# Optimization experiments

Measured on AMD Instinct MI355X. Metric: run time of the kernel, lower is better.

Reference implementation:

```python
import jax, jax.numpy as jnp
import numpy as np

DIM = 1024
HEADS = 8  # hardcoded in original view(batch, N, 3, 8, -1)
HEAD_DIM = DIM // HEADS
# NOTE: original computes self.d = (dim/head_num)**(-0.5) and then divides scores by it,
# which is equivalent to MULTIPLYING scores by sqrt(head_dim). We replicate that exactly.
SCALE = float(np.sqrt(DIM / HEADS))


def setup_inputs() -> dict:
    key = jax.random.key(0)
    k_x, k_w1, k_b1, k_w0, k_b0 = jax.random.split(key, 5)
    B, N = 4, 2048
    bound1 = 1.0 / np.sqrt(DIM)
    x = jax.random.normal(k_x, (B, N, DIM), dtype=jnp.float32)
    # nn.Linear(dim, dim*3): weight [3*dim, dim], bias [3*dim]
    W_qkv = jax.random.uniform(k_w1, (3 * DIM, DIM), jnp.float32, -bound1, bound1)
    b_qkv = jax.random.uniform(k_b1, (3 * DIM,), jnp.float32, -bound1, bound1)
    # nn.Linear(dim, dim)
    W0 = jax.random.uniform(k_w0, (DIM, DIM), jnp.float32, -bound1, bound1)
    b0 = jax.random.uniform(k_b0, (DIM,), jnp.float32, -bound1, bound1)
    return {"x": x, "W_qkv": W_qkv, "b_qkv": b_qkv, "W0": W0, "b0": b0}


def reference(x, W_qkv, b_qkv, W0, b0):
    B, N, C = x.shape
    qkv = jnp.einsum("bnc,oc->bno", x, W_qkv) + b_qkv          # [B,N,3C]
    qkv = qkv.reshape(B, N, 3, HEADS, HEAD_DIM)
    qkv = jnp.transpose(qkv, (2, 0, 3, 1, 4))                   # [3,B,H,N,Dh]
    q, k, v = qkv[0], qkv[1], qkv[2]
    scores = jnp.einsum("bhnd,bhmd->bhnm", q, k) * SCALE        # [B,H,N,N]
    attn = jax.nn.softmax(scores, axis=-1)
    out = jnp.einsum("bhnm,bhmd->bhnd", attn, v)                # [B,H,N,Dh]
    out = jnp.transpose(out, (0, 2, 1, 3)).reshape(B, N, C)
    return jnp.einsum("bnc,oc->bno", out, W0) + b0
```

## Files before the change

### kernel.cpp

```cpp
#include <hip/hip_runtime.h>
#include <hip/hip_bf16.h>

constexpr int DIM   = 1024;
constexpr int HEADS = 8;
constexpr int HD    = 128;
constexpr int SEQ   = 2048;
constexpr int BATCH = 4;
constexpr int BN_ROWS = BATCH * SEQ;
#define SCALE_F 11.3137084989847603904f

typedef __attribute__((ext_vector_type(8))) short  short8;
typedef __attribute__((ext_vector_type(8))) ushort u16x8;
typedef __attribute__((ext_vector_type(4))) float  f32x4;

__device__ __forceinline__ ushort split_hi(float x, float& rem) {
    unsigned xb = __builtin_bit_cast(unsigned, x);
    unsigned hb = xb & 0xFFFF0000u;
    rem = x - __builtin_bit_cast(float, hb);
    return (ushort)(xb >> 16);
}
__device__ __forceinline__ ushort rne16(float x) {
    unsigned xb = __builtin_bit_cast(unsigned, x);
    unsigned r  = xb + 0x7FFFu + ((xb >> 16) & 1u);
    return (ushort)(r >> 16);
}

constexpr int GS = 40;

__global__ __launch_bounds__(256)
void gemm_split_kernel(const float* __restrict__ A, const float* __restrict__ B,
                       const float* __restrict__ bias, float* __restrict__ C,
                       int M, int N, int K)
{
    __shared__ ushort Ah[128 * GS], Al[128 * GS];
    __shared__ ushort Bh[128 * GS], Bl[128 * GS];

    const int tid  = threadIdx.x;
    const int lane = tid & 63;
    const int w    = tid >> 6;
    const int l15  = lane & 15;
    const int g    = lane >> 4;

    const int nbn   = N >> 7;
    const int nb    = (M >> 7) * nbn;
    const int chunk = nb >> 3;
    const int pid   = blockIdx.x;
    const int lb    = (pid & 7) * chunk + (pid >> 3);
    const int m0    = (lb / nbn) * 128;
    const int n0    = (lb % nbn) * 128;

    const int mw = (w >> 1) * 64;
    const int nw = (w & 1) * 64;

    const int srow = tid >> 1;
    const int scol = (tid & 1) * 16;

    f32x4 acc[4][4];
#pragma unroll
    for (int i = 0; i < 4; ++i)
#pragma unroll
        for (int j = 0; j < 4; ++j) acc[i][j] = (f32x4){0.f, 0.f, 0.f, 0.f};

    for (int k0 = 0; k0 < K; k0 += 32) {
        __syncthreads();
        {
            const float* Ap = &A[(size_t)(m0 + srow) * K + k0 + scol];
            const float* Bp = &B[(size_t)(n0 + srow) * K + k0 + scol];
            float av[16], bv[16];
#pragma unroll
            for (int i = 0; i < 4; ++i) {
                *(float4*)&av[i * 4] = *(const float4*)&Ap[i * 4];
                *(float4*)&bv[i * 4] = *(const float4*)&Bp[i * 4];
            }
#pragma unroll
            for (int hlf = 0; hlf < 2; ++hlf) {
                short8 HA, LA, HB, LB;
#pragma unroll
                for (int j = 0; j < 8; ++j) {
                    float r;
                    HA[j] = (short)split_hi(av[hlf * 8 + j], r);
                    LA[j] = (short)rne16(r);
                    HB[j] = (short)split_hi(bv[hlf * 8 + j], r);
                    LB[j] = (short)rne16(r);
                }
                const int off = srow * GS + scol + hlf * 8;
                *(short8*)&Ah[off] = HA;
                *(short8*)&Al[off] = LA;
                *(short8*)&Bh[off] = HB;
                *(short8*)&Bl[off] = LB;
            }
        }
        __syncthreads();

        short8 a_h[4], a_l[4];
#pragma unroll
        for (int mi = 0; mi < 4; ++mi) {
            const int off = (mw + mi * 16 + l15) * GS + g * 8;
            a_h[mi] = *(const short8*)&Ah[off];
            a_l[mi] = *(const short8*)&Al[off];
        }
#pragma unroll
        for (int ni = 0; ni < 4; ++ni) {
            const int off = (nw + ni * 16 + l15) * GS + g * 8;
            short8 b_h = *(const short8*)&Bh[off];
            short8 b_l = *(const short8*)&Bl[off];
#pragma unroll
            for (int mi = 0; mi < 4; ++mi) {
                acc[mi][ni] = __builtin_amdgcn_mfma_f32_16x16x32_bf16(a_h[mi], b_h, acc[mi][ni], 0, 0, 0);
                acc[mi][ni] = __builtin_amdgcn_mfma_f32_16x16x32_bf16(a_l[mi], b_h, acc[mi][ni], 0, 0, 0);
                acc[mi][ni] = __builtin_amdgcn_mfma_f32_16x16x32_bf16(a_h[mi], b_l, acc[mi][ni], 0, 0, 0);
            }
        }
    }

#pragma unroll
    for (int ni = 0; ni < 4; ++ni) {
        const int col = n0 + nw + ni * 16 + l15;
        const float bb = bias[col];
#pragma unroll
        for (int mi = 0; mi < 4; ++mi) {
            const int row = m0 + mw + mi * 16 + 4 * g;
#pragma unroll
            for (int r = 0; r < 4; ++r)
                C[(size_t)(row + r) * N + col] = acc[mi][ni][r] + bb;
        }
    }
}

__global__ __launch_bounds__(256, 2)
void attn_mfma_kernel(const float* __restrict__ qkv, float* __restrict__ outp)
{
    constexpr int QB = 64, KB = 64, NT = SEQ / KB;
    constexpr int VS = 72;
    __shared__ ushort Khi[KB * HD];
    __shared__ ushort Klo[KB * HD];
    __shared__ ushort Vt[HD * VS];
    __shared__ ushort Pl[QB * VS];

    const int tid  = threadIdx.x;
    const int lane = tid & 63;
    const int w    = tid >> 6;
    const int l15  = lane & 15;
    const int g    = lane >> 4;

    const int pid = blockIdx.x;
    const int lb  = (pid & 7) * 128 + (pid >> 3);
    const int qt  = lb & 31;
    const int bh_ = lb >> 5;
    const int h   = bh_ & 7, b = bh_ >> 3;
    const int q0  = qt * QB;

    short8 qh[4], qlo[4];
    {
        const float* qbase =
            &qkv[((size_t)(b * SEQ + q0 + 16 * w + l15) * 3 + 0) * DIM + h * HD];
#pragma unroll
        for (int dc = 0; dc < 4; ++dc) {
            float4 x0 = *(const float4*)&qbase[dc * 32 + g * 8];
            float4 x1 = *(const float4*)&qbase[dc * 32 + g * 8 + 4];
            float xs[8] = {x0.x, x0.y, x0.z, x0.w, x1.x, x1.y, x1.z, x1.w};
            short8 H, L;
#pragma unroll
            for (int j = 0; j < 8; ++j) {
                float r;
                H[j] = (short)split_hi(xs[j], r);
                L[j] = (short)rne16(r);
            }
            qh[dc] = H; qlo[dc] = L;
        }
    }

    const int krow = tid >> 2;
    const int kc0  = (tid & 3) * 32;
    const int vk0  = (tid & 31) * 2;
    const int vd0  = (tid >> 5) * 16;

    const size_t kgbase = ((size_t)(b * SEQ) * 3 + 1) * DIM + h * HD;
    const size_t vgbase = ((size_t)(b * SEQ) * 3 + 2) * DIM + h * HD;

    float4 kld[8], vld[8];
    {
        const float* kp = &qkv[kgbase + (size_t)krow * 3 * DIM + kc0];
#pragma unroll
        for (int i = 0; i < 8; ++i) kld[i] = *(const float4*)&kp[i * 4];
        const float* vp = &qkv[vgbase + (size_t)vk0 * 3 * DIM + vd0];
#pragma unroll
        for (int i = 0; i < 4; ++i) {
            vld[i]     = *(const float4*)&vp[i * 4];
            vld[4 + i] = *(const float4*)&vp[3 * DIM + i * 4];
        }
    }

    float m_st[4], l_st[4];
#pragma unroll
    for (int r = 0; r < 4; ++r) { m_st[r] = -INFINITY; l_st[r] = 0.f; }
    f32x4 o[8];
#pragma unroll
    for (int n = 0; n < 8; ++n) o[n] = (f32x4){0.f, 0.f, 0.f, 0.f};

    const int kmsk = (krow & 15) * 8;

    for (int kt = 0; kt < NT; ++kt) {
#pragma unroll
        for (int c = 0; c < 4; ++c) {
            const float* kx = (const float*)&kld[c * 2];
            short8 H, L;
#pragma unroll
            for (int j = 0; j < 8; ++j) {
                float r;
                H[j] = (short)split_hi(kx[j], r);
                L[j] = (short)rne16(r);
            }
            const int off = krow * HD + ((kc0 + c * 8) ^ kmsk);
            *(short8*)&Khi[off] = H;
            *(short8*)&Klo[off] = L;
        }
        {
            const float* va = (const float*)&vld[0];
            const float* vb = (const float*)&vld[4];
#pragma unroll
            for (int i = 0; i < 16; ++i) {
                unsigned pk = (unsigned)rne16(va[i]) | ((unsigned)rne16(vb[i]) << 16);
                *(unsigned*)&Vt[(vd0 + i) * VS + vk0] = pk;
            }
        }
        __syncthreads();

        if (kt + 1 < NT) {
            const float* kp = &qkv[kgbase + (size_t)((kt + 1) * KB + krow) * 3 * DIM + kc0];
#pragma unroll
            for (int i = 0; i < 8; ++i) kld[i] = *(const float4*)&kp[i * 4];
            const float* vp = &qkv[vgbase + (size_t)((kt + 1) * KB + vk0) * 3 * DIM + vd0];
#pragma unroll
            for (int i = 0; i < 4; ++i) {
                vld[i]     = *(const float4*)&vp[i * 4];
                vld[4 + i] = *(const float4*)&vp[3 * DIM + i * 4];
            }
        }

        f32x4 sacc[4];
#pragma unroll
        for (int n = 0; n < 4; ++n) sacc[n] = (f32x4){0.f, 0.f, 0.f, 0.f};
        __builtin_amdgcn_s_setprio(1);
#pragma unroll
        for (int dc = 0; dc < 4; ++dc) {
            const int sw = (dc * 32 + g * 8) ^ (l15 * 8);
#pragma unroll
            for (int n = 0; n < 4; ++n) {
                const int off = (n * 16 + l15) * HD + sw;
                short8 kh = *(const short8*)&Khi[off];
                short8 kl = *(const short8*)&Klo[off];
                sacc[n] = __builtin_amdgcn_mfma_f32_16x16x32_bf16(qh[dc], kh, sacc[n], 0, 0, 0);
                sacc[n] = __builtin_amdgcn_mfma_f32_16x16x32_bf16(qh[dc], kl, sacc[n], 0, 0, 0);
                sacc[n] = __builtin_amdgcn_mfma_f32_16x16x32_bf16(qlo[dc], kh, sacc[n], 0, 0, 0);
            }
        }
        __builtin_amdgcn_s_setprio(0);

        float alpha[4];
#pragma unroll
        for (int r = 0; r < 4; ++r) {
            float s0 = sacc[0][r] * SCALE_F;
            float s1 = sacc[1][r] * SCALE_F;
            float s2 = sacc[2][r] * SCALE_F;
            float s3 = sacc[3][r] * SCALE_F;
            float mx = fmaxf(fmaxf(s0, s1), fmaxf(s2, s3));
            mx = fmaxf(mx, __shfl_xor(mx, 1));
            mx = fmaxf(mx, __shfl_xor(mx, 2));
            mx = fmaxf(mx, __shfl_xor(mx, 4));
            mx = fmaxf(mx, __shfl_xor(mx, 8));
            const float mnew = fmaxf(m_st[r], mx);
            alpha[r] = __expf(m_st[r] - mnew);
            const float p0 = __expf(s0 - mnew);
            const float p1 = __expf(s1 - mnew);
            const float p2 = __expf(s2 - mnew);
            const float p3 = __expf(s3 - mnew);
            const int prow = (16 * w + 4 * g + r) * VS;
            Pl[prow + l15]      = rne16(p0);
            Pl[prow + 16 + l15] = rne16(p1);
            Pl[prow + 32 + l15] = rne16(p2);
            Pl[prow + 48 + l15] = rne16(p3);
            float ps = (p0 + p1) + (p2 + p3);
            ps += __shfl_xor(ps, 1);
            ps += __shfl_xor(ps, 2);
            ps += __shfl_xor(ps, 4);
            ps += __shfl_xor(ps, 8);
            l_st[r] = l_st[r] * alpha[r] + ps;
            m_st[r] = mnew;
        }
#pragma unroll
        for (int n = 0; n < 8; ++n)
#pragma unroll
            for (int r = 0; r < 4; ++r) o[n][r] *= alpha[r];

        __builtin_amdgcn_s_setprio(1);
#pragma unroll
        for (int ks = 0; ks < 2; ++ks) {
            short8 pa = *(const short8*)&Pl[(16 * w + l15) * VS + ks * 32 + g * 8];
#pragma unroll
            for (int n = 0; n < 8; ++n) {
                short8 vbf = *(const short8*)&Vt[(n * 16 + l15) * VS + ks * 32 + g * 8];
                o[n] = __builtin_amdgcn_mfma_f32_16x16x32_bf16(pa, vbf, o[n], 0, 0, 0);
            }
        }
        __builtin_amdgcn_s_setprio(0);
        __syncthreads();
    }

    float rl[4];
#pragma unroll
    for (int r = 0; r < 4; ++r) rl[r] = 1.f / l_st[r];
    const size_t orow0 = (size_t)(b * SEQ + q0 + 16 * w + 4 * g);
#pragma unroll
    for (int n = 0; n < 8; ++n)
#pragma unroll
        for (int r = 0; r < 4; ++r)
            outp[(orow0 + r) * DIM + h * HD + n * 16 + l15] = o[n][r] * rl[r];
}

extern "C" void kernel_launch(void* const* d_in, const int* in_sizes, int n_in,
                              void* d_out, int out_size, void* d_ws, size_t ws_size,
                              hipStream_t stream)
{
    const float* x     = (const float*)d_in[0];
    const float* W_qkv = (const float*)d_in[1];
    const float* b_qkv = (const float*)d_in[2];
    const float* W0    = (const float*)d_in[3];
    const float* b0    = (const float*)d_in[4];
    float* out = (float*)d_out;

    float* qkv  = (float*)d_ws;
    float* attn = (float*)((char*)d_ws + (size_t)BN_ROWS * 3 * DIM * 4);

    gemm_split_kernel<<<dim3((BN_ROWS / 128) * (3 * DIM / 128)), 256, 0, stream>>>(
        x, W_qkv, b_qkv, qkv, BN_ROWS, 3 * DIM, DIM);

    attn_mfma_kernel<<<dim3(BATCH * HEADS * (SEQ / 64)), 256, 0, stream>>>(qkv, attn);

    gemm_split_kernel<<<dim3((BN_ROWS / 128) * (DIM / 128)), 256, 0, stream>>>(
        attn, W0, b0, out, BN_ROWS, DIM, DIM);
}
```

Baseline: 602.1 us.

## Emit pre-split bf16 Q/K and transposed V from QKV GEMM, async-load in attention

```diff
diff --git a/kernel.cpp b/kernel.cpp
--- a/kernel.cpp
+++ b/kernel.cpp
@@ -10,7 +10,6 @@
 #define SCALE_F 11.3137084989847603904f
 
 typedef __attribute__((ext_vector_type(8))) short  short8;
-typedef __attribute__((ext_vector_type(8))) ushort u16x8;
 typedef __attribute__((ext_vector_type(4))) float  f32x4;
 
 __device__ __forceinline__ ushort split_hi(float x, float& rem) {
@@ -24,117 +23,161 @@
     unsigned r  = xb + 0x7FFFu + ((xb >> 16) & 1u);
     return (ushort)(r >> 16);
 }
+__device__ __forceinline__ void gload16(const void* g, void* l) {
+    __builtin_amdgcn_global_load_lds(
+        (const __attribute__((address_space(1))) void*)g,
+        (__attribute__((address_space(3))) void*)l, 16, 0, 0);
+}
 
 constexpr int GS = 40;
+
+#define GEMM_BODY(EPILOGUE)                                                      \
+    __shared__ ushort Ah[128 * GS], Al[128 * GS];                                \
+    __shared__ ushort Bh[128 * GS], Bl[128 * GS];                                \
+    const int tid  = threadIdx.x;                                                \
+    const int lane = tid & 63;                                                   \
+    const int w    = tid >> 6;                                                   \
+    const int l15  = lane & 15;                                                  \
+    const int g    = lane >> 4;                                                  \
+    const int nbn   = N >> 7;                                                    \
+    const int nb    = (M >> 7) * nbn;                                            \
+    const int chunk = nb >> 3;                                                   \
+    const int pid   = blockIdx.x;                                                \
+    const int lb    = (pid & 7) * chunk + (pid >> 3);                            \
+    const int m0    = (lb / nbn) * 128;                                          \
+    const int n0    = (lb % nbn) * 128;                                          \
+    const int mw = (w >> 1) * 64;                                                \
+    const int nw = (w & 1) * 64;                                                 \
+    const int srow = tid >> 1;                                                   \
+    const int scol = (tid & 1) * 16;                                             \
+    f32x4 acc[4][4];                                                             \
+    _Pragma("unroll") for (int i = 0; i < 4; ++i)                                \
+        _Pragma("unroll") for (int j = 0; j < 4; ++j)                            \
+            acc[i][j] = (f32x4){0.f, 0.f, 0.f, 0.f};                             \
+    for (int k0 = 0; k0 < K; k0 += 32) {                                         \
+        __syncthreads();                                                         \
+        {                                                                        \
+            const float* Ap = &A[(size_t)(m0 + srow) * K + k0 + scol];           \
+            const float* Bp = &B[(size_t)(n0 + srow) * K + k0 + scol];           \
+            float av[16], bv[16];                                                \
+            _Pragma("unroll") for (int i = 0; i < 4; ++i) {                      \
+                *(float4*)&av[i * 4] = *(const float4*)&Ap[i * 4];               \
+                *(float4*)&bv[i * 4] = *(const float4*)&Bp[i * 4];               \
+            }                                                                    \
+            _Pragma("unroll") for (int hlf = 0; hlf < 2; ++hlf) {                \
+                short8 HA, LA, HB, LB;                                           \
+                _Pragma("unroll") for (int j = 0; j < 8; ++j) {                  \
+                    float r;                                                     \
+                    HA[j] = (short)split_hi(av[hlf * 8 + j], r);                 \
+                    LA[j] = (short)rne16(r);                                     \
+                    HB[j] = (short)split_hi(bv[hlf * 8 + j], r);                 \
+                    LB[j] = (short)rne16(r);                                     \
+                }                                                                \
+                const int off = srow * GS + scol + hlf * 8;                      \
+                *(short8*)&Ah[off] = HA;                                         \
+                *(short8*)&Al[off] = LA;                                         \
+                *(short8*)&Bh[off] = HB;                                         \
+                *(short8*)&Bl[off] = LB;                                         \
+            }                                                                    \
+        }                                                                        \
+        __syncthreads();                                                         \
+        short8 a_h[4], a_l[4];                                                   \
+        _Pragma("unroll") for (int mi = 0; mi < 4; ++mi) {                       \
+            const int off = (mw + mi * 16 + l15) * GS + g * 8;                   \
+            a_h[mi] = *(const short8*)&Ah[off];                                  \
+            a_l[mi] = *(const short8*)&Al[off];                                  \
+        }                                                                        \
+        _Pragma("unroll") for (int ni = 0; ni < 4; ++ni) {                       \
+            const int off = (nw + ni * 16 + l15) * GS + g * 8;                   \
+            short8 b_h = *(const short8*)&Bh[off];                               \
+            short8 b_l = *(const short8*)&Bl[off];                               \
+            _Pragma("unroll") for (int mi = 0; mi < 4; ++mi) {                   \
+                acc[mi][ni] = __builtin_amdgcn_mfma_f32_16x16x32_bf16(a_h[mi], b_h, acc[mi][ni], 0, 0, 0); \
+                acc[mi][ni] = __builtin_amdgcn_mfma_f32_16x16x32_bf16(a_l[mi], b_h, acc[mi][ni], 0, 0, 0); \
+                acc[mi][ni] = __builtin_amdgcn_mfma_f32_16x16x32_bf16(a_h[mi], b_l, acc[mi][ni], 0, 0, 0); \
+            }                                                                    \
+        }                                                                        \
+    }                                                                            \
+    EPILOGUE
 
 __global__ __launch_bounds__(256)
 void gemm_split_kernel(const float* __restrict__ A, const float* __restrict__ B,
                        const float* __restrict__ bias, float* __restrict__ C,
                        int M, int N, int K)
 {
-    __shared__ ushort Ah[128 * GS], Al[128 * GS];
-    __shared__ ushort Bh[128 * GS], Bl[128 * GS];
-
-    const int tid  = threadIdx.x;
-    const int lane = tid & 63;
-    const int w    = tid >> 6;
-    const int l15  = lane & 15;
-    const int g    = lane >> 4;
-
-    const int nbn   = N >> 7;
-    const int nb    = (M >> 7) * nbn;
-    const int chunk = nb >> 3;
-    const int pid   = blockIdx.x;
-    const int lb    = (pid & 7) * chunk + (pid >> 3);
-    const int m0    = (lb / nbn) * 128;
-    const int n0    = (lb % nbn) * 128;
-
-    const int mw = (w >> 1) * 64;
-    const int nw = (w & 1) * 64;
-
-    const int srow = tid >> 1;
-    const int scol = (tid & 1) * 16;
-
-    f32x4 acc[4][4];
-#pragma unroll
-    for (int i = 0; i < 4; ++i)
-#pragma unroll
-        for (int j = 0; j < 4; ++j) acc[i][j] = (f32x4){0.f, 0.f, 0.f, 0.f};
-
-    for (int k0 = 0; k0 < K; k0 += 32) {
-        __syncthreads();
-        {
-            const float* Ap = &A[(size_t)(m0 + srow) * K + k0 + scol];
-            const float* Bp = &B[(size_t)(n0 + srow) * K + k0 + scol];
-            float av[16], bv[16];
-#pragma unroll
-            for (int i = 0; i < 4; ++i) {
-                *(float4*)&av[i * 4] = *(const float4*)&Ap[i * 4];
-                *(float4*)&bv[i * 4] = *(const float4*)&Bp[i * 4];
-            }
-#pragma unroll
-            for (int hlf = 0; hlf < 2; ++hlf) {
-                short8 HA, LA, HB, LB;
-#pragma unroll
-                for (int j = 0; j < 8; ++j) {
-                    float r;
-                    HA[j] = (short)split_hi(av[hlf * 8 + j], r);
-                    LA[j] = (short)rne16(r);
-                    HB[j] = (short)split_hi(bv[hlf * 8 + j], r);
-                    LB[j] = (short)rne16(r);
+    GEMM_BODY({
+        _Pragma("unroll") for (int ni = 0; ni < 4; ++ni) {
+            const int col = n0 + nw + ni * 16 + l15;
+            const float bb = bias[col];
+            _Pragma("unroll") for (int mi = 0; mi < 4; ++mi) {
+                const int row = m0 + mw + mi * 16 + 4 * g;
+                _Pragma("unroll") for (int r = 0; r < 4; ++r)
+                    C[(size_t)(row + r) * N + col] = acc[mi][ni][r] + bb;
+            }
+        }
+    })
+}
+
+__global__ __launch_bounds__(256)
+void gemm_qkv_kernel(const float* __restrict__ A, const float* __restrict__ B,
+                     const float* __restrict__ bias,
+                     ushort* __restrict__ Qhi_g, ushort* __restrict__ Qlo_g,
+                     ushort* __restrict__ Khi_g, ushort* __restrict__ Klo_g,
+                     ushort* __restrict__ Vt_g,
+                     int M, int N, int K)
+{
+    GEMM_BODY({
+        const int kind = n0 >> 10;
+        const int colbase = (n0 & 1023) + nw;
+        if (kind < 2) {
+            ushort* hi_g = (kind == 0) ? Qhi_g : Khi_g;
+            ushort* lo_g = (kind == 0) ? Qlo_g : Klo_g;
+            _Pragma("unroll") for (int ni = 0; ni < 4; ++ni) {
+                const int colp = colbase + ni * 16 + l15;
+                const float bb = bias[n0 + nw + ni * 16 + l15];
+                _Pragma("unroll") for (int mi = 0; mi < 4; ++mi) {
+                    const int row = m0 + mw + mi * 16 + 4 * g;
+                    _Pragma("unroll") for (int r = 0; r < 4; ++r) {
+                        float rem;
+                        const float y = acc[mi][ni][r] + bb;
+                        const ushort hb = split_hi(y, rem);
+                        const ushort lb = rne16(rem);
+                        const size_t idx = (size_t)(row + r) * DIM + colp;
+                        hi_g[idx] = hb;
+                        lo_g[idx] = lb;
+                    }
                 }
-                const int off = srow * GS + scol + hlf * 8;
-                *(short8*)&Ah[off] = HA;
-                *(short8*)&Al[off] = LA;
-                *(short8*)&Bh[off] = HB;
-                *(short8*)&Bl[off] = LB;
-            }
-        }
-        __syncthreads();
-
-        short8 a_h[4], a_l[4];
-#pragma unroll
-        for (int mi = 0; mi < 4; ++mi) {
-            const int off = (mw + mi * 16 + l15) * GS + g * 8;
-            a_h[mi] = *(const short8*)&Ah[off];
-            a_l[mi] = *(const short8*)&Al[off];
-        }
-#pragma unroll
-        for (int ni = 0; ni < 4; ++ni) {
-            const int off = (nw + ni * 16 + l15) * GS + g * 8;
-            short8 b_h = *(const short8*)&Bh[off];
-            short8 b_l = *(const short8*)&Bl[off];
-#pragma unroll
-            for (int mi = 0; mi < 4; ++mi) {
-                acc[mi][ni] = __builtin_amdgcn_mfma_f32_16x16x32_bf16(a_h[mi], b_h, acc[mi][ni], 0, 0, 0);
-                acc[mi][ni] = __builtin_amdgcn_mfma_f32_16x16x32_bf16(a_l[mi], b_h, acc[mi][ni], 0, 0, 0);
-                acc[mi][ni] = __builtin_amdgcn_mfma_f32_16x16x32_bf16(a_h[mi], b_l, acc[mi][ni], 0, 0, 0);
-            }
-        }
-    }
-
-#pragma unroll
-    for (int ni = 0; ni < 4; ++ni) {
-        const int col = n0 + nw + ni * 16 + l15;
-        const float bb = bias[col];
-#pragma unroll
-        for (int mi = 0; mi < 4; ++mi) {
-            const int row = m0 + mw + mi * 16 + 4 * g;
-#pragma unroll
-            for (int r = 0; r < 4; ++r)
-                C[(size_t)(row + r) * N + col] = acc[mi][ni][r] + bb;
-        }
-    }
-}
-
-__global__ __launch_bounds__(256, 2)
-void attn_mfma_kernel(const float* __restrict__ qkv, float* __restrict__ outp)
+            }
+        } else {
+            _Pragma("unroll") for (int ni = 0; ni < 4; ++ni) {
+                const int colp = colbase + ni * 16 + l15;
+                const float bb = bias[n0 + nw + ni * 16 + l15];
+                _Pragma("unroll") for (int mi = 0; mi < 4; ++mi) {
+                    const int row0 = m0 + mw + mi * 16 + 4 * g;
+                    const unsigned p01 = (unsigned)rne16(acc[mi][ni][0] + bb)
+                                       | ((unsigned)rne16(acc[mi][ni][1] + bb) << 16);
+                    const unsigned p23 = (unsigned)rne16(acc[mi][ni][2] + bb)
+                                       | ((unsigned)rne16(acc[mi][ni][3] + bb) << 16);
+                    const size_t idx = ((size_t)((row0 >> 11) * 1024 + colp)) * SEQ
+                                     + (row0 & 2047);
+                    uint2 pk; pk.x = p01; pk.y = p23;
+                    *(uint2*)&Vt_g[idx] = pk;
+                }
+            }
+        }
+    })
+}
+
+__global__ __launch_bounds__(256, 3)
+void attn_mfma_kernel(const ushort* __restrict__ Qhi_g, const ushort* __restrict__ Qlo_g,
+                      const ushort* __restrict__ Khi_g, const ushort* __restrict__ Klo_g,
+                      const ushort* __restrict__ Vt_g, float* __restrict__ outp)
 {
-    constexpr int QB = 64, KB = 64, NT = SEQ / KB;
-    constexpr int VS = 72;
-    __shared__ ushort Khi[KB * HD];
-    __shared__ ushort Klo[KB * HD];
-    __shared__ ushort Vt[HD * VS];
+    constexpr int QB = 64, KB = 32, NT = SEQ / KB;
+    constexpr int VS = 40;
+    __shared__ ushort KhiL[2][KB * HD];
+    __shared__ ushort KloL[2][KB * HD];
+    __shared__ ushort VtL[2][HD * KB];
     __shared__ ushort Pl[QB * VS];
 
     const int tid  = threadIdx.x;
@@ -152,42 +195,30 @@
 
     short8 qh[4], qlo[4];
     {
-        const float* qbase =
-            &qkv[((size_t)(b * SEQ + q0 + 16 * w + l15) * 3 + 0) * DIM + h * HD];
+        const size_t qoff = (size_t)(b * SEQ + q0 + 16 * w + l15) * DIM + h * HD;
 #pragma unroll
         for (int dc = 0; dc < 4; ++dc) {
-            float4 x0 = *(const float4*)&qbase[dc * 32 + g * 8];
-            float4 x1 = *(const float4*)&qbase[dc * 32 + g * 8 + 4];
-            float xs[8] = {x0.x, x0.y, x0.z, x0.w, x1.x, x1.y, x1.z, x1.w};
-            short8 H, L;
-#pragma unroll
-            for (int j = 0; j < 8; ++j) {
-                float r;
-                H[j] = (short)split_hi(xs[j], r);
-                L[j] = (short)rne16(r);
-            }
-            qh[dc] = H; qlo[dc] = L;
+            qh[dc]  = *(const short8*)&Qhi_g[qoff + dc * 32 + g * 8];
+            qlo[dc] = *(const short8*)&Qlo_g[qoff + dc * 32 + g * 8];
         }
     }
 
-    const int krow = tid >> 2;
-    const int kc0  = (tid & 3) * 32;
-    const int vk0  = (tid & 31) * 2;
-    const int vd0  = (tid >> 5) * 16;
-
-    const size_t kgbase = ((size_t)(b * SEQ) * 3 + 1) * DIM + h * HD;
-    const size_t vgbase = ((size_t)(b * SEQ) * 3 + 2) * DIM + h * HD;
-
-    float4 kld[8], vld[8];
+    const ushort* kph[2]; const ushort* kpl[2]; const ushort* vpp[2];
     {
-        const float* kp = &qkv[kgbase + (size_t)krow * 3 * DIM + kc0];
-#pragma unroll
-        for (int i = 0; i < 8; ++i) kld[i] = *(const float4*)&kp[i * 4];
-        const float* vp = &qkv[vgbase + (size_t)vk0 * 3 * DIM + vd0];
-#pragma unroll
-        for (int i = 0; i < 4; ++i) {
-            vld[i]     = *(const float4*)&vp[i * 4];
-            vld[4 + i] = *(const float4*)&vp[3 * DIM + i * 4];
+        const int kcol = l15 * 8;
+#pragma unroll
+        for (int i = 0; i < 2; ++i) {
+            const int r_loc = 8 * w + 4 * i + g;
+            const int sc    = kcol ^ ((r_loc & 15) * 8);
+            const size_t off = (size_t)(b * SEQ + r_loc) * DIM + h * HD + sc;
+            kph[i] = Khi_g + off;
+            kpl[i] = Klo_g + off;
+        }
+#pragma unroll
+        for (int i = 0; i < 2; ++i) {
+            const int d_loc = 32 * w + 16 * i + (lane >> 2);
+            const int scv   = ((lane & 3) * 8) ^ ((d_loc & 3) * 8);
+            vpp[i] = Vt_g + (size_t)((b * HEADS + h) * HD + d_loc) * SEQ + scv;
         }
     }
 
@@ -198,58 +229,41 @@
 #pragma unroll
     for (int n = 0; n < 8; ++n) o[n] = (f32x4){0.f, 0.f, 0.f, 0.f};
 
-    const int kmsk = (krow & 15) * 8;
+#pragma unroll
+    for (int i = 0; i < 2; ++i) {
+        gload16(kph[i], &KhiL[0][(8 * w + 4 * i) * HD]);
+        gload16(kpl[i], &KloL[0][(8 * w + 4 * i) * HD]);
+        gload16(vpp[i], &VtL[0][(32 * w + 16 * i) * KB]);
+        kph[i] += (size_t)KB * DIM; kpl[i] += (size_t)KB * DIM; vpp[i] += KB;
+    }
 
     for (int kt = 0; kt < NT; ++kt) {
-#pragma unroll
-        for (int c = 0; c < 4; ++c) {
-            const float* kx = (const float*)&kld[c * 2];
-            short8 H, L;
-#pragma unroll
-            for (int j = 0; j < 8; ++j) {
-                float r;
-                H[j] = (short)split_hi(kx[j], r);
-                L[j] = (short)rne16(r);
-            }
-            const int off = krow * HD + ((kc0 + c * 8) ^ kmsk);
-            *(short8*)&Khi[off] = H;
-            *(short8*)&Klo[off] = L;
-        }
-        {
-            const float* va = (const float*)&vld[0];
-            const float* vb = (const float*)&vld[4];
-#pragma unroll
-            for (int i = 0; i < 16; ++i) {
-                unsigned pk = (unsigned)rne16(va[i]) | ((unsigned)rne16(vb[i]) << 16);
-                *(unsigned*)&Vt[(vd0 + i) * VS + vk0] = pk;
-            }
-        }
+        const int cur = kt & 1;
         __syncthreads();
 
         if (kt + 1 < NT) {
-            const float* kp = &qkv[kgbase + (size_t)((kt + 1) * KB + krow) * 3 * DIM + kc0];
-#pragma unroll
-            for (int i = 0; i < 8; ++i) kld[i] = *(const float4*)&kp[i * 4];
-            const float* vp = &qkv[vgbase + (size_t)((kt + 1) * KB + vk0) * 3 * DIM + vd0];
-#pragma unroll
-            for (int i = 0; i < 4; ++i) {
-                vld[i]     = *(const float4*)&vp[i * 4];
-                vld[4 + i] = *(const float4*)&vp[3 * DIM + i * 4];
-            }
-        }
-
-        f32x4 sacc[4];
-#pragma unroll
-        for (int n = 0; n < 4; ++n) sacc[n] = (f32x4){0.f, 0.f, 0.f, 0.f};
+            const int nxt = cur ^ 1;
+#pragma unroll
+            for (int i = 0; i < 2; ++i) {
+                gload16(kph[i], &KhiL[nxt][(8 * w + 4 * i) * HD]);
+                gload16(kpl[i], &KloL[nxt][(8 * w + 4 * i) * HD]);
+                gload16(vpp[i], &VtL[nxt][(32 * w + 16 * i) * KB]);
+                kph[i] += (size_t)KB * DIM; kpl[i] += (size_t)KB * DIM; vpp[i] += KB;
+            }
+        }
+
+        f32x4 sacc[2];
+        sacc[0] = (f32x4){0.f, 0.f, 0.f, 0.f};
+        sacc[1] = (f32x4){0.f, 0.f, 0.f, 0.f};
         __builtin_amdgcn_s_setprio(1);
 #pragma unroll
         for (int dc = 0; dc < 4; ++dc) {
             const int sw = (dc * 32 + g * 8) ^ (l15 * 8);
 #pragma unroll
-            for (int n = 0; n < 4; ++n) {
+            for (int n = 0; n < 2; ++n) {
                 const int off = (n * 16 + l15) * HD + sw;
-                short8 kh = *(const short8*)&Khi[off];
-                short8 kl = *(const short8*)&Klo[off];
+                short8 kh = *(const short8*)&KhiL[cur][off];
+                short8 kl = *(const short8*)&KloL[cur][off];
                 sacc[n] = __builtin_amdgcn_mfma_f32_16x16x32_bf16(qh[dc], kh, sacc[n], 0, 0, 0);
                 sacc[n] = __builtin_amdgcn_mfma_f32_16x16x32_bf16(qh[dc], kl, sacc[n], 0, 0, 0);
                 sacc[n] = __builtin_amdgcn_mfma_f32_16x16x32_bf16(qlo[dc], kh, sacc[n], 0, 0, 0);
@@ -262,9 +276,7 @@
         for (int r = 0; r < 4; ++r) {
             float s0 = sacc[0][r] * SCALE_F;
             float s1 = sacc[1][r] * SCALE_F;
-            float s2 = sacc[2][r] * SCALE_F;
-            float s3 = sacc[3][r] * SCALE_F;
-            float mx = fmaxf(fmaxf(s0, s1), fmaxf(s2, s3));
+            float mx = fmaxf(s0, s1);
             mx = fmaxf(mx, __shfl_xor(mx, 1));
             mx = fmaxf(mx, __shfl_xor(mx, 2));
             mx = fmaxf(mx, __shfl_xor(mx, 4));
@@ -273,14 +285,10 @@
             alpha[r] = __expf(m_st[r] - mnew);
             const float p0 = __expf(s0 - mnew);
             const float p1 = __expf(s1 - mnew);
-            const float p2 = __expf(s2 - mnew);
-            const float p3 = __expf(s3 - mnew);
             const int prow = (16 * w + 4 * g + r) * VS;
             Pl[prow + l15]      = rne16(p0);
             Pl[prow + 16 + l15] = rne16(p1);
-            Pl[prow + 32 + l15] = rne16(p2);
-            Pl[prow + 48 + l15] = rne16(p3);
-            float ps = (p0 + p1) + (p2 + p3);
+            float ps = p0 + p1;
             ps += __shfl_xor(ps, 1);
             ps += __shfl_xor(ps, 2);
             ps += __shfl_xor(ps, 4);
@@ -294,17 +302,14 @@
             for (int r = 0; r < 4; ++r) o[n][r] *= alpha[r];
 
         __builtin_amdgcn_s_setprio(1);
-#pragma unroll
-        for (int ks = 0; ks < 2; ++ks) {
-            short8 pa = *(const short8*)&Pl[(16 * w + l15) * VS + ks * 32 + g * 8];
-#pragma unroll
-            for (int n = 0; n < 8; ++n) {
-                short8 vbf = *(const short8*)&Vt[(n * 16 + l15) * VS + ks * 32 + g * 8];
-                o[n] = __builtin_amdgcn_mfma_f32_16x16x32_bf16(pa, vbf, o[n], 0, 0, 0);
-            }
+        short8 pa = *(const short8*)&Pl[(16 * w + l15) * VS + g * 8];
+#pragma unroll
+        for (int n = 0; n < 8; ++n) {
+            const int vrow = n * 16 + l15;
+            short8 vbf = *(const short8*)&VtL[cur][vrow * KB + ((g * 8) ^ ((l15 & 3) * 8))];
+            o[n] = __builtin_amdgcn_mfma_f32_16x16x32_bf16(pa, vbf, o[n], 0, 0, 0);
         }
         __builtin_amdgcn_s_setprio(0);
-        __syncthreads();
     }
 
     float rl[4];
@@ -329,13 +334,19 @@
     const float* b0    = (const float*)d_in[4];
     float* out = (float*)d_out;
 
-    float* qkv  = (float*)d_ws;
-    float* attn = (float*)((char*)d_ws + (size_t)BN_ROWS * 3 * DIM * 4);
-
-    gemm_split_kernel<<<dim3((BN_ROWS / 128) * (3 * DIM / 128)), 256, 0, stream>>>(
-        x, W_qkv, b_qkv, qkv, BN_ROWS, 3 * DIM, DIM);
-
-    attn_mfma_kernel<<<dim3(BATCH * HEADS * (SEQ / 64)), 256, 0, stream>>>(qkv, attn);
+    const size_t PL = (size_t)BN_ROWS * DIM;
+    ushort* Qhi = (ushort*)d_ws;
+    ushort* Qlo = Qhi + PL;
+    ushort* Khi = Qhi + 2 * PL;
+    ushort* Klo = Qhi + 3 * PL;
+    ushort* Vt  = Qhi + 4 * PL;
+    float*  attn = (float*)(Qhi + 5 * PL);
+
+    gemm_qkv_kernel<<<dim3((BN_ROWS / 128) * (3 * DIM / 128)), 256, 0, stream>>>(
+        x, W_qkv, b_qkv, Qhi, Qlo, Khi, Klo, Vt, BN_ROWS, 3 * DIM, DIM);
+
+    attn_mfma_kernel<<<dim3(BATCH * HEADS * (SEQ / 64)), 256, 0, stream>>>(
+        Qhi, Qlo, Khi, Klo, Vt, attn);
 
     gemm_split_kernel<<<dim3((BN_ROWS / 128) * (DIM / 128)), 256, 0, stream>>>(
         attn, W0, b0, out, BN_ROWS, DIM, DIM);
```

Measured after the change: 609.3 us. About the same (+1.2%).
